# Kernel optimization log

Measured on AMD Instinct MI355X. Metric: run time of the kernel, lower is better.

The kernel has to match this reference:

```python
import jax, jax.numpy as jnp
import numpy as np

IN_DIM = 128
OUT_DIM = 128
NUM_INTERVALS = 8
SPLINE_ORDER = 3
BATCH = 1024


def make_grids():
    # domain [-1, 1] for every (in, out) pair, extended by spline_order knots each side
    step = 2.0 / NUM_INTERVALS
    G = NUM_INTERVALS + 2 * SPLINE_ORDER + 1
    g = (-1.0 - SPLINE_ORDER * step) + jnp.arange(G, dtype=jnp.float32) * step  # [G]
    return jnp.broadcast_to(g, (IN_DIM, OUT_DIM, G))


def setup_inputs() -> dict:
    key = jax.random.key(0)
    k1, k2, k3 = jax.random.split(key, 3)
    x = jax.random.normal(k1, (BATCH, IN_DIM), dtype=jnp.float32)
    n_cp = NUM_INTERVALS + SPLINE_ORDER
    control_points = 0.1 * jax.random.normal(k2, (IN_DIM, OUT_DIM, n_cp), dtype=jnp.float32)
    scaling_factors = np.sqrt(2.0 / OUT_DIM).astype(np.float32) * jax.random.normal(
        k3, (IN_DIM, OUT_DIM), dtype=jnp.float32)
    grids = make_grids()
    return {"x": x, "control_points": control_points,
            "scaling_factors": scaling_factors, "grids": grids}


def bspline_bases(x, grids, k):
    # Bottom-up Cox-de-Boor DP (identical recurrence to the naive top-down version).
    # x: [B, in], grids: [in, out, G] -> returns all degree-k bases [B, in, out, G-1-k]
    ex = x[:, :, None, None]          # [B, in, 1, 1]
    t = grids[None]                   # [1, in, out, G]
    B = ((t[..., :-1] <= ex) & (ex < t[..., 1:])).astype(x.dtype)  # degree 0
    for d in range(1, k + 1):
        tl  = t[..., : -(d + 1)]      # t[i]
        tr  = t[..., d:-1]            # t[i+d]
        tl1 = t[..., 1:-d]            # t[i+1]
        tr1 = t[..., d + 1:]          # t[i+d+1]
        B = (ex - tl) / (tr - tl) * B[..., :-1] + (tr1 - ex) / (tr1 - tl1) * B[..., 1:]
    return B


def reference(x, control_points, scaling_factors, grids):
    Bk = bspline_bases(x, grids, SPLINE_ORDER)                 # [B, in, out, n_cp]
    spline = jnp.einsum('biog,iog->bio', Bk, control_points)    # [B, in, out]
    res = scaling_factors[None] * (jax.nn.silu(x)[:, :, None] + spline)
    return jnp.sum(res, axis=1).astype(jnp.float32)             # [B, out]
```

## Files before the change

kernel.cpp:

```cpp
#include <hip/hip_runtime.h>
#include <math.h>


#define IN_DIM   128
#define OUT_DIM  128
#define NCP      11
#define GK       15
#define BT       8
#define OT       32
#define KS       8
#define THREADS  256
#define FS       12

__global__ __launch_bounds__(THREADS, 2)
void kan_fused(const float* __restrict__ X,
               const float* __restrict__ CP,
               const float* __restrict__ SF,
               const float* __restrict__ GR,
               float* __restrict__ OUT)
{
    __shared__ float F[BT * IN_DIM * FS];

    const int tid = threadIdx.x;
    const int b0  = blockIdx.x * BT;
    const int o0  = blockIdx.y * OT;

    const float t0 = GR[0];
    const float h  = GR[1] - t0;
    const float r1 = 1.0f / h;
    const float r2 = 1.0f / (2.0f * h);
    const float r3 = 1.0f / (3.0f * h);
    float kn[GK];
    #pragma unroll
    for (int j = 0; j < GK; ++j) kn[j] = t0 + (float)j * h;

    #pragma unroll
    for (int k = 0; k < (BT * IN_DIM) / THREADS; ++k) {
        const int p = tid + k * THREADS;
        const int r = p >> 7;
        const int i = p & (IN_DIM - 1);

        const float x = X[(b0 + r) * IN_DIM + i];

        float b[GK - 1];
        #pragma unroll
        for (int j = 0; j < GK - 1; ++j)
            b[j] = (kn[j] <= x && x < kn[j + 1]) ? 1.0f : 0.0f;

        #pragma unroll
        for (int j = 0; j < GK - 2; ++j)
            b[j] = ((x - kn[j]) * b[j] + (kn[j + 2] - x) * b[j + 1]) * r1;
        #pragma unroll
        for (int j = 0; j < GK - 3; ++j)
            b[j] = ((x - kn[j]) * b[j] + (kn[j + 3] - x) * b[j + 1]) * r2;
        #pragma unroll
        for (int j = 0; j < GK - 4; ++j)
            b[j] = ((x - kn[j]) * b[j] + (kn[j + 4] - x) * b[j + 1]) * r3;

        const float silu = x / (1.0f + __expf(-x));

        float* f = &F[p * FS];
        #pragma unroll
        for (int g = 0; g < NCP; ++g) f[g] = b[g];
        f[NCP] = silu;
    }
    __syncthreads();

    const int ol = tid & (OT - 1);
    const int ks = tid >> 5;
    const int o  = o0 + ol;

    float acc[BT];
    #pragma unroll
    for (int r = 0; r < BT; ++r) acc[r] = 0.0f;

    const int i0 = ks * (IN_DIM / KS);

    for (int i = i0; i < i0 + (IN_DIM / KS); ++i) {
        const float s  = SF[i * OUT_DIM + o];
        const float* cp = CP + (i * OUT_DIM + o) * NCP;
        float w[NCP];
        #pragma unroll
        for (int g = 0; g < NCP; ++g) w[g] = cp[g];

        const float* fb = &F[i * FS];
        #pragma unroll
        for (int r = 0; r < BT; ++r) {
            const float* f = fb + r * IN_DIM * FS;
            float t = f[NCP];
            #pragma unroll
            for (int g = 0; g < NCP; ++g)
                t = fmaf(w[g], f[g], t);
            acc[r] = fmaf(s, t, acc[r]);
        }
    }

    __syncthreads();
    if (ks > 0) {
        #pragma unroll
        for (int r = 0; r < BT; ++r)
            F[((ks - 1) * BT + r) * OT + ol] = acc[r];
    }
    __syncthreads();
    if (ks == 0) {
        #pragma unroll
        for (int r = 0; r < BT; ++r) {
            float v = acc[r];
            #pragma unroll
            for (int q = 0; q < KS - 1; ++q)
                v += F[(q * BT + r) * OT + ol];
            OUT[(b0 + r) * OUT_DIM + o] = v;
        }
    }
}

extern "C" void kernel_launch(void* const* d_in, const int* in_sizes, int n_in,
                              void* d_out, int out_size, void* d_ws, size_t ws_size,
                              hipStream_t stream) {
    const float* x  = (const float*)d_in[0];
    const float* cp = (const float*)d_in[1];
    const float* sf = (const float*)d_in[2];
    const float* gr = (const float*)d_in[3];
    float* out = (float*)d_out;

    const int batch = in_sizes[0] / IN_DIM;
    dim3 grid(batch / BT, OUT_DIM / OT);
    kan_fused<<<grid, THREADS, 0, stream>>>(x, cp, sf, gr, out);
}
```

Measured before the change: 76.33 us.

## Pre-scale control points into K-major weight matrix and vectorize GEMM-style inner loop

Adds a prep kernel that folds the scaling factors into the control points and writes them transposed as a [IN*FS, OUT] matrix in workspace, so the main kernel reads weights with coalesced per-output loads instead of strided 11-float chunks per thread. The main loop becomes a plain dot product over a flattened K dimension, reading float4 features from shared memory, and the launch bound is raised to 3 blocks per CU. The cost is an extra kernel launch and a workspace round trip on every call.

Measured after the change: 76.61 us. No clear change (+0.4%).

```diff
diff --git a/kernel.cpp b/kernel.cpp
--- a/kernel.cpp
+++ b/kernel.cpp
@@ -6,20 +6,37 @@
 #define OUT_DIM  128
 #define NCP      11
 #define GK       15
+#define FS       12
+#define KTOT     (IN_DIM * FS)
 #define BT       8
 #define OT       32
 #define KS       8
 #define THREADS  256
-#define FS       12
 
-__global__ __launch_bounds__(THREADS, 2)
-void kan_fused(const float* __restrict__ X,
-               const float* __restrict__ CP,
-               const float* __restrict__ SF,
-               const float* __restrict__ GR,
-               float* __restrict__ OUT)
+__global__ __launch_bounds__(256)
+void kan_prep(const float* __restrict__ CP,
+              const float* __restrict__ SF,
+              float* __restrict__ W)
 {
-    __shared__ float F[BT * IN_DIM * FS];
+    const int p = blockIdx.x * 256 + threadIdx.x;
+    const int i = p >> 7;
+    const int o = p & (OUT_DIM - 1);
+    const float s = SF[p];
+    const float* cp = CP + p * NCP;
+    const int kb = i * FS;
+    #pragma unroll
+    for (int g = 0; g < NCP; ++g)
+        W[(kb + g) * OUT_DIM + o] = s * cp[g];
+    W[(kb + NCP) * OUT_DIM + o] = s;
+}
+
+__global__ __launch_bounds__(THREADS, 3)
+void kan_main(const float* __restrict__ X,
+              const float* __restrict__ GR,
+              const float* __restrict__ W,
+              float* __restrict__ OUT)
+{
+    __shared__ float F[BT * KTOT];
 
     const int tid = threadIdx.x;
     const int b0  = blockIdx.x * BT;
@@ -35,8 +52,8 @@
     for (int j = 0; j < GK; ++j) kn[j] = t0 + (float)j * h;
 
     #pragma unroll
-    for (int k = 0; k < (BT * IN_DIM) / THREADS; ++k) {
-        const int p = tid + k * THREADS;
+    for (int kq = 0; kq < (BT * IN_DIM) / THREADS; ++kq) {
+        const int p = tid + kq * THREADS;
         const int r = p >> 7;
         const int i = p & (IN_DIM - 1);
 
@@ -46,7 +63,6 @@
         #pragma unroll
         for (int j = 0; j < GK - 1; ++j)
             b[j] = (kn[j] <= x && x < kn[j + 1]) ? 1.0f : 0.0f;
-
         #pragma unroll
         for (int j = 0; j < GK - 2; ++j)
             b[j] = ((x - kn[j]) * b[j] + (kn[j + 2] - x) * b[j + 1]) * r1;
@@ -59,7 +75,7 @@
 
         const float silu = x / (1.0f + __expf(-x));
 
-        float* f = &F[p * FS];
+        float* f = &F[r * KTOT + i * FS];
         #pragma unroll
         for (int g = 0; g < NCP; ++g) f[g] = b[g];
         f[NCP] = silu;
@@ -74,24 +90,21 @@
     #pragma unroll
     for (int r = 0; r < BT; ++r) acc[r] = 0.0f;
 
-    const int i0 = ks * (IN_DIM / KS);
-
-    for (int i = i0; i < i0 + (IN_DIM / KS); ++i) {
-        const float s  = SF[i * OUT_DIM + o];
-        const float* cp = CP + (i * OUT_DIM + o) * NCP;
-        float w[NCP];
-        #pragma unroll
-        for (int g = 0; g < NCP; ++g) w[g] = cp[g];
-
-        const float* fb = &F[i * FS];
+    const int kbase = ks * (KTOT / KS);
+    #pragma unroll 2
+    for (int kk = 0; kk < KTOT / KS; kk += 4) {
+        const int k = kbase + kk;
+        const float w0 = W[(k + 0) * OUT_DIM + o];
+        const float w1 = W[(k + 1) * OUT_DIM + o];
+        const float w2 = W[(k + 2) * OUT_DIM + o];
+        const float w3 = W[(k + 3) * OUT_DIM + o];
         #pragma unroll
         for (int r = 0; r < BT; ++r) {
-            const float* f = fb + r * IN_DIM * FS;
-            float t = f[NCP];
-            #pragma unroll
-            for (int g = 0; g < NCP; ++g)
-                t = fmaf(w[g], f[g], t);
-            acc[r] = fmaf(s, t, acc[r]);
+            const float4 f = *(const float4*)&F[r * KTOT + k];
+            acc[r] = fmaf(w0, f.x, acc[r]);
+            acc[r] = fmaf(w1, f.y, acc[r]);
+            acc[r] = fmaf(w2, f.z, acc[r]);
+            acc[r] = fmaf(w3, f.w, acc[r]);
         }
     }
 
@@ -122,8 +135,11 @@
     const float* sf = (const float*)d_in[2];
     const float* gr = (const float*)d_in[3];
     float* out = (float*)d_out;
+    float* W   = (float*)d_ws;
 
     const int batch = in_sizes[0] / IN_DIM;
+
+    kan_prep<<<(IN_DIM * OUT_DIM) / 256, 256, 0, stream>>>(cp, sf, W);
     dim3 grid(batch / BT, OUT_DIM / OT);
-    kan_fused<<<grid, THREADS, 0, stream>>>(x, cp, sf, gr, out);
+    kan_main<<<grid, THREADS, 0, stream>>>(x, gr, W, out);
 }
```
